# Kernel tuning notes

Measured on AMD Instinct MI355X. Metric: run time of the kernel, lower is better.

Reference implementation:

```python
import jax, jax.numpy as jnp
import numpy as np

EMBED_DIM = 1024
NUM_HEADS = 16
HEAD_DIM = EMBED_DIM // NUM_HEADS
B, S = 2, 2048
NEG = -1e20


def setup_inputs() -> dict:
    key = jax.random.key(0)
    ks = jax.random.split(key, 8)
    scale = 0.02
    return {
        "query": jax.random.normal(ks[0], (B, S, EMBED_DIM), jnp.float32),
        "keys": jax.random.normal(ks[1], (B, S, EMBED_DIM), jnp.float32),
        "values": jax.random.normal(ks[2], (B, S, EMBED_DIM), jnp.float32),
        "mask": jax.random.randint(ks[3], (1, 1, S, S), 0, 2, jnp.int32),
        "Wq": jax.random.normal(ks[4], (EMBED_DIM, EMBED_DIM), jnp.float32) * scale,
        "Wk": jax.random.normal(ks[5], (EMBED_DIM, EMBED_DIM), jnp.float32) * scale,
        "Wv": jax.random.normal(ks[6], (EMBED_DIM, EMBED_DIM), jnp.float32) * scale,
        "Wo": jax.random.normal(ks[7], (EMBED_DIM, EMBED_DIM), jnp.float32) * scale,
        "bo": jnp.zeros((EMBED_DIM,), jnp.float32),
    }


def reference(query, keys, values, mask, Wq, Wk, Wv, Wo, bo):
    N, Lq, _ = query.shape
    Lk = keys.shape[1]
    # torch nn.Linear: y = x @ W.T  (bias=False for Q/K/V)
    Q = (query @ Wq.T).reshape(N, Lq, NUM_HEADS, HEAD_DIM)
    K = (keys @ Wk.T).reshape(N, Lk, NUM_HEADS, HEAD_DIM)
    V = (values @ Wv.T).reshape(N, Lk, NUM_HEADS, HEAD_DIM)
    # NOTE: source scales by sqrt(embed_dim), not sqrt(head_dim) — kept faithful.
    energy = jnp.einsum("nqhd,nkhd->nhqk", Q, K) / jnp.sqrt(
        jnp.asarray(EMBED_DIM, Q.dtype)
    )
    energy = jnp.where(mask == 0, jnp.asarray(NEG, energy.dtype), energy)
    attention = jax.nn.softmax(energy, axis=3)
    out = jnp.einsum("nhqk,nkhd->nqhd", attention, V).reshape(N, Lq, EMBED_DIM)
    return out @ Wo.T + bo
```

## Files before the change

### kernel.cpp

```cpp
#include <hip/hip_runtime.h>
#include <stdint.h>

typedef __bf16 bf16;
typedef __bf16 bf16x4 __attribute__((ext_vector_type(4)));
typedef __bf16 bf16x8 __attribute__((ext_vector_type(8)));
typedef float f32x4 __attribute__((ext_vector_type(4)));
typedef float f32x16 __attribute__((ext_vector_type(16)));

#define MFMA16(a, b, c) __builtin_amdgcn_mfma_f32_16x16x32_bf16((a), (b), (c), 0, 0, 0)
#define MFMA32(a, b, c) __builtin_amdgcn_mfma_f32_32x32x16_bf16((a), (b), (c), 0, 0, 0)

__device__ __forceinline__ void gload16(const bf16* g, bf16* l) {
    __builtin_amdgcn_global_load_lds(
        (const __attribute__((address_space(1))) void*)g,
        (__attribute__((address_space(3))) void*)l, 16, 0, 0);
}

__global__ __launch_bounds__(256) void cvt_kernel(
    const float* __restrict__ q, const float* __restrict__ k, const float* __restrict__ v,
    const float* __restrict__ wq, const float* __restrict__ wk,
    const float* __restrict__ wv, const float* __restrict__ wo,
    bf16* __restrict__ qb, bf16* __restrict__ kb, bf16* __restrict__ vb,
    bf16* __restrict__ wqb, bf16* __restrict__ wkb, bf16* __restrict__ wvb,
    bf16* __restrict__ wob)
{
    int z = blockIdx.z;
    const float* src; bf16* dst; int n;
    switch (z) {
        case 0:  src = q;  dst = qb;  n = 4194304; break;
        case 1:  src = k;  dst = kb;  n = 4194304; break;
        case 2:  src = v;  dst = vb;  n = 4194304; break;
        case 3:  src = wq; dst = wqb; n = 1048576; break;
        case 4:  src = wk; dst = wkb; n = 1048576; break;
        case 5:  src = wv; dst = wvb; n = 1048576; break;
        default: src = wo; dst = wob; n = 1048576; break;
    }
    int i = (blockIdx.x * 256 + threadIdx.x) * 8;
    if (i >= n) return;
    float4 f0 = *(const float4*)(src + i);
    float4 f1 = *(const float4*)(src + i + 4);
    bf16x8 o;
    o[0] = (bf16)f0.x; o[1] = (bf16)f0.y; o[2] = (bf16)f0.z; o[3] = (bf16)f0.w;
    o[4] = (bf16)f1.x; o[5] = (bf16)f1.y; o[6] = (bf16)f1.z; o[7] = (bf16)f1.w;
    *(bf16x8*)(dst + i) = o;
}

__global__ __launch_bounds__(256) void maskpack_kernel(
    const int* __restrict__ mask, unsigned long long* __restrict__ maskb)
{
    int gid  = blockIdx.x * 256 + threadIdx.x;
    int word = gid >> 6;
    int lane = gid & 63;
    int row = word >> 5, wc = word & 31;
    int mv = mask[row * 2048 + wc * 64 + lane];
    unsigned long long bits = __ballot(mv != 0);
    if (lane == 0) maskb[word] = bits;
}

template <int OUTMODE, int MT>
__global__ __launch_bounds__(256) void gemm_kernel(
    const bf16* __restrict__ A0, const bf16* __restrict__ A1, const bf16* __restrict__ A2,
    const bf16* __restrict__ B0, const bf16* __restrict__ B1, const bf16* __restrict__ B2,
    bf16* __restrict__ C0, bf16* __restrict__ C1, bf16* __restrict__ C2,
    const float* __restrict__ bias, float* __restrict__ outf)
{
    constexpr int MI = (MT == 128) ? 4 : 2;

    const int z = blockIdx.z;
    const bf16* A = (z == 0) ? A0 : (z == 1) ? A1 : A2;
    const bf16* B = (z == 0) ? B0 : (z == 1) ? B1 : B2;

    __shared__ bf16 At[MT * 32];
    __shared__ bf16 Bt[128 * 32];

    const int tid  = threadIdx.x;
    const int lane = tid & 63;
    const int wave = tid >> 6;
    const int quad = lane >> 4;
    const int l16  = lane & 15;
    const int wm = (wave >> 1) * (MT / 2);
    const int wn = (wave & 1) * 64;
    const int m0 = blockIdx.y * MT;
    const int n0 = blockIdx.x * 128;

    const int lrow = lane >> 2;
    const int lcol = (lane & 3) * 8;

    f32x4 acc[MI][4] = {};

    const bf16* Ag = A + (size_t)(m0 + lrow) * 1024 + lcol;
    const bf16* Bg = B + (size_t)(n0 + lrow) * 1024 + lcol;

    for (int k0 = 0; k0 < 1024; k0 += 32) {
        __syncthreads();
        if constexpr (MT == 128) {
#pragma unroll
            for (int j = 0; j < 2; ++j)
                gload16(Ag + (size_t)(wave * 32 + j * 16) * 1024 + k0,
                        At + (wave * 32 + j * 16) * 32);
        } else {
            gload16(Ag + (size_t)(wave * 16) * 1024 + k0, At + (wave * 16) * 32);
        }
#pragma unroll
        for (int j = 0; j < 2; ++j)
            gload16(Bg + (size_t)(wave * 32 + j * 16) * 1024 + k0,
                    Bt + (wave * 32 + j * 16) * 32);
        __syncthreads();

        bf16x8 af[MI], bg[4];
#pragma unroll
        for (int i = 0; i < MI; ++i)
            af[i] = *(const bf16x8*)(At + (wm + i * 16 + l16) * 32 + quad * 8);
#pragma unroll
        for (int j = 0; j < 4; ++j)
            bg[j] = *(const bf16x8*)(Bt + (wn + j * 16 + l16) * 32 + quad * 8);
#pragma unroll
        for (int i = 0; i < MI; ++i)
#pragma unroll
            for (int j = 0; j < 4; ++j)
                acc[i][j] = MFMA16(af[i], bg[j], acc[i][j]);
    }

    if constexpr (OUTMODE == 0) {
        bf16* C = (z == 0) ? C0 : (z == 1) ? C1 : C2;
        const float cs = (z == 0) ? 0.03125f : 1.0f;
#pragma unroll
        for (int i = 0; i < MI; ++i)
#pragma unroll
            for (int j = 0; j < 4; ++j) {
                int row = m0 + wm + i * 16 + quad * 4;
                int col = n0 + wn + j * 16 + l16;
#pragma unroll
                for (int r = 0; r < 4; ++r)
                    C[(row + r) * 1024 + col] = (bf16)(acc[i][j][r] * cs);
            }
    } else {
#pragma unroll
        for (int j = 0; j < 4; ++j) {
            int col = n0 + wn + j * 16 + l16;
            float bj = bias[col];
#pragma unroll
            for (int i = 0; i < MI; ++i) {
                int row = m0 + wm + i * 16 + quad * 4;
#pragma unroll
                for (int r = 0; r < 4; ++r)
                    outf[(row + r) * 1024 + col] = acc[i][j][r] + bj;
            }
        }
    }
}

__global__ __launch_bounds__(256) void transpose_kernel(const bf16* __restrict__ V,
                                                        bf16* __restrict__ Vt)
{
    __shared__ bf16 t[64][72];
    const int tid = threadIdx.x;
    const int b  = blockIdx.z;
    const int s0 = blockIdx.x * 64;
    const int d0 = blockIdx.y * 64;
#pragma unroll
    for (int c = 0; c < 2; ++c) {
        int qq = c * 256 + tid;
        int row = qq >> 3, col = (qq & 7) * 8;
        *(uint4*)(&t[row][col]) =
            *(const uint4*)(V + (size_t)(b * 2048 + s0 + row) * 1024 + d0 + col);
    }
    __syncthreads();
#pragma unroll
    for (int c = 0; c < 2; ++c) {
        int qq = c * 256 + tid;
        int drow = qq >> 3, scol = (qq & 7) * 8;
        bf16x8 o;
#pragma unroll
        for (int j = 0; j < 8; ++j) o[j] = t[scol + j][drow];
        *(bf16x8*)(Vt + (size_t)(b * 1024 + d0 + drow) * 2048 + s0 + scol) = o;
    }
}

__global__ __launch_bounds__(256) void flash_kernel(
    const bf16* __restrict__ Q, const bf16* __restrict__ K, const bf16* __restrict__ Vt,
    const unsigned long long* __restrict__ maskb, bf16* __restrict__ O)
{
    __shared__ bf16 Kl[64 * 64];
    __shared__ bf16 Vl[64 * 64];
    __shared__ bf16 Pl[128 * 72];

    const int tid  = threadIdx.x;
    const int lane = tid & 63;
    const int wave = tid >> 6;
    const int l32  = lane & 31;
    const int hl   = lane >> 5;
    const int l7   = lane & 7;
    const int b  = blockIdx.z;
    const int h  = blockIdx.y;
    const int q0 = blockIdx.x * 128;
    const int qt = q0 + wave * 32;

    const bf16* Qb = Q + (size_t)(b * 2048 + qt + l32) * 1024 + h * 64 + hl * 8;
    bf16x8 qf[4];
#pragma unroll
    for (int ks = 0; ks < 4; ++ks) qf[ks] = *(const bf16x8*)(Qb + ks * 16);

    bf16x8 ones;
#pragma unroll
    for (int j = 0; j < 8; ++j) ones[j] = (bf16)1.0f;

    f32x16 acc[2] = {};
    f32x16 lacc = {};

    const int dmarow = lane >> 3;
    const int dmacol = (l7 ^ dmarow) * 8;
    const bf16* Kg = K + (size_t)(b * 2048 + wave * 16 + dmarow) * 1024 + h * 64 + dmacol;
    const bf16* Vg = Vt + (size_t)((b * 16 + h) * 64 + wave * 16 + dmarow) * 2048 + dmacol;
    bf16* Kw = Kl + (wave * 16) * 64;
    bf16* Vw = Vl + (wave * 16) * 64;
    const unsigned long long* Mg = maskb + (size_t)(qt + l32) * 32;

    bf16* Pq = Pl + (wave * 32 + l32) * 72;

    for (int kt = 0; kt < 2048; kt += 64) {
        unsigned long long mw = Mg[kt >> 6];
        __syncthreads();
        gload16(Kg + (size_t)kt * 1024,       Kw);
        gload16(Kg + (size_t)(kt + 8) * 1024, Kw + 8 * 64);
        gload16(Vg + kt,                      Vw);
        gload16(Vg + kt + 8 * 2048,           Vw + 8 * 64);
        __syncthreads();

#pragma unroll
        for (int t = 0; t < 2; ++t) {
            f32x16 s = {};
#pragma unroll
            for (int ks = 0; ks < 4; ++ks) {
                bf16x8 ka = *(const bf16x8*)(Kl + (t * 32 + l32) * 64 +
                                             (((ks * 2 + hl) ^ l7) * 8));
                s = MFMA32(ka, qf[ks], s);
            }
            unsigned long long mwt = mw >> (t * 32 + 4 * hl);
#pragma unroll
            for (int g = 0; g < 4; ++g) {
                bf16x4 pv;
#pragma unroll
                for (int r = 0; r < 4; ++r) {
                    bool keep = (mwt >> (8 * g + r)) & 1ULL;
                    float e = __expf(s[g * 4 + r]);
                    pv[r] = keep ? (bf16)e : (bf16)0.0f;
                }
                *(bf16x4*)(Pq + t * 32 + 4 * hl + 8 * g) = pv;
            }
        }

        bf16x8 pa[4];
#pragma unroll
        for (int ks = 0; ks < 4; ++ks)
            pa[ks] = *(const bf16x8*)(Pq + ks * 16 + hl * 8);
#pragma unroll
        for (int dt = 0; dt < 2; ++dt)
#pragma unroll
            for (int ks = 0; ks < 4; ++ks) {
                bf16x8 vb = *(const bf16x8*)(Vl + (dt * 32 + l32) * 64 +
                                             (((ks * 2 + hl) ^ l7) * 8));
                acc[dt] = MFMA32(pa[ks], vb, acc[dt]);
            }
#pragma unroll
        for (int ks = 0; ks < 4; ++ks)
            lacc = MFMA32(pa[ks], ones, lacc);
    }

    const size_t obase = (size_t)(b * 2048 + qt) * 1024 + h * 64;
#pragma unroll
    for (int g = 0; g < 4; ++g)
#pragma unroll
        for (int r = 0; r < 4; ++r) {
            int qr = 4 * hl + 8 * g + r;
            float inv = 1.0f / lacc[g * 4 + r];
            O[obase + (size_t)qr * 1024 + l32]      = (bf16)(acc[0][g * 4 + r] * inv);
            O[obase + (size_t)qr * 1024 + 32 + l32] = (bf16)(acc[1][g * 4 + r] * inv);
        }
}

extern "C" void kernel_launch(void* const* d_in, const int* in_sizes, int n_in,
                              void* d_out, int out_size, void* d_ws, size_t ws_size,
                              hipStream_t stream)
{
    const float* q  = (const float*)d_in[0];
    const float* k  = (const float*)d_in[1];
    const float* v  = (const float*)d_in[2];
    const int* mask = (const int*)d_in[3];
    const float* wq = (const float*)d_in[4];
    const float* wk = (const float*)d_in[5];
    const float* wv = (const float*)d_in[6];
    const float* wo = (const float*)d_in[7];
    const float* bo = (const float*)d_in[8];
    float* out = (float*)d_out;

    char* p = (char*)d_ws;
    auto alloc = [&](size_t bytes) {
        char* r = p;
        p += (bytes + 255) & ~(size_t)255;
        return r;
    };
    const size_t SB = (size_t)4096 * 1024 * 2;
    const size_t WB = (size_t)1024 * 1024 * 2;
    bf16* qb  = (bf16*)alloc(SB);
    bf16* kb  = (bf16*)alloc(SB);
    bf16* vb  = (bf16*)alloc(SB);
    bf16* wqb = (bf16*)alloc(WB);
    bf16* wkb = (bf16*)alloc(WB);
    bf16* wvb = (bf16*)alloc(WB);
    bf16* wob = (bf16*)alloc(WB);
    bf16* Qp  = (bf16*)alloc(SB);
    bf16* Kp  = (bf16*)alloc(SB);
    bf16* Vp  = (bf16*)alloc(SB);
    bf16* Vtp = (bf16*)alloc(SB);
    bf16* Ob  = (bf16*)alloc(SB);
    unsigned long long* maskb = (unsigned long long*)alloc(2048 * 32 * 8);

    cvt_kernel<<<dim3(2048, 1, 7), 256, 0, stream>>>(
        q, k, v, wq, wk, wv, wo, qb, kb, vb, wqb, wkb, wvb, wob);

    maskpack_kernel<<<dim3(16384), 256, 0, stream>>>(mask, maskb);

    gemm_kernel<0, 128><<<dim3(8, 32, 3), 256, 0, stream>>>(
        qb, kb, vb, wqb, wkb, wvb, Qp, Kp, Vp, nullptr, nullptr);

    transpose_kernel<<<dim3(32, 16, 2), 256, 0, stream>>>(Vp, Vtp);

    flash_kernel<<<dim3(16, 16, 2), 256, 0, stream>>>(Qp, Kp, Vtp, maskb, Ob);

    gemm_kernel<1, 64><<<dim3(8, 64, 1), 256, 0, stream>>>(
        Ob, nullptr, nullptr, wob, nullptr, nullptr,
        nullptr, nullptr, nullptr, bo, out);
}
```

Before: 255.3 us.

## Fuse V transpose into GEMM epilogue and split flash keys across waves

The V projection GEMM now writes its output directly in transposed layout, which removes the separate transpose kernel and its intermediate buffer. The flash kernel shrinks its query tile to 64 rows and doubles the grid. Each pair of waves now splits every 64-key block into two 32-key halves, and the partial outputs and row sums are reduced through shared memory at the end. The Q scale folds in log2(e) so exp2f can replace __expf, and launch bounds request higher occupancy. The cost is extra K/V tile loads per query, an end-of-kernel shared-memory reduction, and uncoalesced 4-element stores in the transposed epilogue.

```diff
diff --git a/kernel.cpp b/kernel.cpp
--- a/kernel.cpp
+++ b/kernel.cpp
@@ -122,18 +122,33 @@
     }
 
     if constexpr (OUTMODE == 0) {
-        bf16* C = (z == 0) ? C0 : (z == 1) ? C1 : C2;
-        const float cs = (z == 0) ? 0.03125f : 1.0f;
-#pragma unroll
-        for (int i = 0; i < MI; ++i)
-#pragma unroll
-            for (int j = 0; j < 4; ++j) {
-                int row = m0 + wm + i * 16 + quad * 4;
-                int col = n0 + wn + j * 16 + l16;
-#pragma unroll
-                for (int r = 0; r < 4; ++r)
-                    C[(row + r) * 1024 + col] = (bf16)(acc[i][j][r] * cs);
-            }
+        if (z == 2) {
+#pragma unroll
+            for (int i = 0; i < MI; ++i)
+#pragma unroll
+                for (int j = 0; j < 4; ++j) {
+                    int row = m0 + wm + i * 16 + quad * 4;
+                    int col = n0 + wn + j * 16 + l16;
+                    bf16x4 pv;
+#pragma unroll
+                    for (int r = 0; r < 4; ++r) pv[r] = (bf16)acc[i][j][r];
+                    *(bf16x4*)(C2 + ((size_t)((row >> 11) * 1024 + col)) * 2048 +
+                               (row & 2047)) = pv;
+                }
+        } else {
+            bf16* C = (z == 0) ? C0 : C1;
+            const float cs = (z == 0) ? 0.04508422f : 1.0f;
+#pragma unroll
+            for (int i = 0; i < MI; ++i)
+#pragma unroll
+                for (int j = 0; j < 4; ++j) {
+                    int row = m0 + wm + i * 16 + quad * 4;
+                    int col = n0 + wn + j * 16 + l16;
+#pragma unroll
+                    for (int r = 0; r < 4; ++r)
+                        C[(row + r) * 1024 + col] = (bf16)(acc[i][j][r] * cs);
+                }
+        }
     } else {
 #pragma unroll
         for (int j = 0; j < 4; ++j) {
@@ -150,40 +165,16 @@
     }
 }
 
-__global__ __launch_bounds__(256) void transpose_kernel(const bf16* __restrict__ V,
-                                                        bf16* __restrict__ Vt)
-{
-    __shared__ bf16 t[64][72];
-    const int tid = threadIdx.x;
-    const int b  = blockIdx.z;
-    const int s0 = blockIdx.x * 64;
-    const int d0 = blockIdx.y * 64;
-#pragma unroll
-    for (int c = 0; c < 2; ++c) {
-        int qq = c * 256 + tid;
-        int row = qq >> 3, col = (qq & 7) * 8;
-        *(uint4*)(&t[row][col]) =
-            *(const uint4*)(V + (size_t)(b * 2048 + s0 + row) * 1024 + d0 + col);
-    }
-    __syncthreads();
-#pragma unroll
-    for (int c = 0; c < 2; ++c) {
-        int qq = c * 256 + tid;
-        int drow = qq >> 3, scol = (qq & 7) * 8;
-        bf16x8 o;
-#pragma unroll
-        for (int j = 0; j < 8; ++j) o[j] = t[scol + j][drow];
-        *(bf16x8*)(Vt + (size_t)(b * 1024 + d0 + drow) * 2048 + s0 + scol) = o;
-    }
-}
-
-__global__ __launch_bounds__(256) void flash_kernel(
+__global__ __launch_bounds__(256, 4) void flash_kernel(
     const bf16* __restrict__ Q, const bf16* __restrict__ K, const bf16* __restrict__ Vt,
     const unsigned long long* __restrict__ maskb, bf16* __restrict__ O)
 {
-    __shared__ bf16 Kl[64 * 64];
-    __shared__ bf16 Vl[64 * 64];
-    __shared__ bf16 Pl[128 * 72];
+    __shared__ char smem[8192 + 8192 + 9216];
+    bf16* Kl = (bf16*)smem;
+    bf16* Vl = (bf16*)(smem + 8192);
+    bf16* Pl = (bf16*)(smem + 16384);
+    float* Obuf = (float*)smem;
+    float* Lbuf = (float*)(smem + 16384);
 
     const int tid  = threadIdx.x;
     const int lane = tid & 63;
@@ -191,10 +182,12 @@
     const int l32  = lane & 31;
     const int hl   = lane >> 5;
     const int l7   = lane & 7;
+    const int qtw  = wave & 1;
+    const int kh   = wave >> 1;
     const int b  = blockIdx.z;
     const int h  = blockIdx.y;
-    const int q0 = blockIdx.x * 128;
-    const int qt = q0 + wave * 32;
+    const int q0 = blockIdx.x * 64;
+    const int qt = q0 + qtw * 32;
 
     const bf16* Qb = Q + (size_t)(b * 2048 + qt + l32) * 1024 + h * 64 + hl * 8;
     bf16x8 qf[4];
@@ -216,7 +209,7 @@
     bf16* Vw = Vl + (wave * 16) * 64;
     const unsigned long long* Mg = maskb + (size_t)(qt + l32) * 32;
 
-    bf16* Pq = Pl + (wave * 32 + l32) * 72;
+    bf16* Pq = Pl + wave * (32 * 36) + l32 * 36;
 
     for (int kt = 0; kt < 2048; kt += 64) {
         unsigned long long mw = Mg[kt >> 6];
@@ -227,56 +220,79 @@
         gload16(Vg + kt + 8 * 2048,           Vw + 8 * 64);
         __syncthreads();
 
-#pragma unroll
-        for (int t = 0; t < 2; ++t) {
-            f32x16 s = {};
-#pragma unroll
-            for (int ks = 0; ks < 4; ++ks) {
-                bf16x8 ka = *(const bf16x8*)(Kl + (t * 32 + l32) * 64 +
-                                             (((ks * 2 + hl) ^ l7) * 8));
-                s = MFMA32(ka, qf[ks], s);
-            }
-            unsigned long long mwt = mw >> (t * 32 + 4 * hl);
-#pragma unroll
-            for (int g = 0; g < 4; ++g) {
-                bf16x4 pv;
-#pragma unroll
-                for (int r = 0; r < 4; ++r) {
-                    bool keep = (mwt >> (8 * g + r)) & 1ULL;
-                    float e = __expf(s[g * 4 + r]);
-                    pv[r] = keep ? (bf16)e : (bf16)0.0f;
-                }
-                *(bf16x4*)(Pq + t * 32 + 4 * hl + 8 * g) = pv;
-            }
-        }
-
-        bf16x8 pa[4];
-#pragma unroll
-        for (int ks = 0; ks < 4; ++ks)
+        f32x16 s = {};
+#pragma unroll
+        for (int ks = 0; ks < 4; ++ks) {
+            bf16x8 ka = *(const bf16x8*)(Kl + (kh * 32 + l32) * 64 +
+                                         (((ks * 2 + hl) ^ l7) * 8));
+            s = MFMA32(ka, qf[ks], s);
+        }
+
+        unsigned long long mq = mw >> (kh * 32 + 4 * hl);
+#pragma unroll
+        for (int g = 0; g < 4; ++g) {
+            bf16x4 pv;
+#pragma unroll
+            for (int r = 0; r < 4; ++r) {
+                bool keep = (mq >> (8 * g + r)) & 1ULL;
+                float e = exp2f(s[g * 4 + r]);
+                pv[r] = keep ? (bf16)e : (bf16)0.0f;
+            }
+            *(bf16x4*)(Pq + 4 * hl + 8 * g) = pv;
+        }
+
+        bf16x8 pa[2];
+#pragma unroll
+        for (int ks = 0; ks < 2; ++ks)
             pa[ks] = *(const bf16x8*)(Pq + ks * 16 + hl * 8);
 #pragma unroll
         for (int dt = 0; dt < 2; ++dt)
 #pragma unroll
-            for (int ks = 0; ks < 4; ++ks) {
+            for (int ks = 0; ks < 2; ++ks) {
                 bf16x8 vb = *(const bf16x8*)(Vl + (dt * 32 + l32) * 64 +
-                                             (((ks * 2 + hl) ^ l7) * 8));
+                                             (((kh * 4 + ks * 2 + hl) ^ l7) * 8));
                 acc[dt] = MFMA32(pa[ks], vb, acc[dt]);
             }
-#pragma unroll
-        for (int ks = 0; ks < 4; ++ks)
-            lacc = MFMA32(pa[ks], ones, lacc);
-    }
-
-    const size_t obase = (size_t)(b * 2048 + qt) * 1024 + h * 64;
-#pragma unroll
-    for (int g = 0; g < 4; ++g)
-#pragma unroll
-        for (int r = 0; r < 4; ++r) {
-            int qr = 4 * hl + 8 * g + r;
-            float inv = 1.0f / lacc[g * 4 + r];
-            O[obase + (size_t)qr * 1024 + l32]      = (bf16)(acc[0][g * 4 + r] * inv);
-            O[obase + (size_t)qr * 1024 + 32 + l32] = (bf16)(acc[1][g * 4 + r] * inv);
-        }
+        lacc = MFMA32(pa[0], ones, lacc);
+        lacc = MFMA32(pa[1], ones, lacc);
+    }
+
+    __syncthreads();
+    if (kh == 1) {
+        float* ob = Obuf + (qtw * 32) * 64;
+#pragma unroll
+        for (int g = 0; g < 4; ++g)
+#pragma unroll
+            for (int r = 0; r < 4; ++r) {
+                int qr = 4 * hl + 8 * g + r;
+                ob[qr * 64 + l32]      = acc[0][g * 4 + r];
+                ob[qr * 64 + 32 + l32] = acc[1][g * 4 + r];
+            }
+        if (l32 == 0) {
+#pragma unroll
+            for (int g = 0; g < 4; ++g)
+#pragma unroll
+                for (int r = 0; r < 4; ++r)
+                    Lbuf[qtw * 32 + 4 * hl + 8 * g + r] = lacc[g * 4 + r];
+        }
+    }
+    __syncthreads();
+    if (kh == 0) {
+        const float* ob = Obuf + (qtw * 32) * 64;
+        const size_t obase = (size_t)(b * 2048 + qt) * 1024 + h * 64;
+#pragma unroll
+        for (int g = 0; g < 4; ++g)
+#pragma unroll
+            for (int r = 0; r < 4; ++r) {
+                int qr = 4 * hl + 8 * g + r;
+                float l = lacc[g * 4 + r] + Lbuf[qtw * 32 + qr];
+                float inv = 1.0f / l;
+                float o0 = acc[0][g * 4 + r] + ob[qr * 64 + l32];
+                float o1 = acc[1][g * 4 + r] + ob[qr * 64 + 32 + l32];
+                O[obase + (size_t)qr * 1024 + l32]      = (bf16)(o0 * inv);
+                O[obase + (size_t)qr * 1024 + 32 + l32] = (bf16)(o1 * inv);
+            }
+    }
 }
 
 extern "C" void kernel_launch(void* const* d_in, const int* in_sizes, int n_in,
@@ -311,7 +327,6 @@
     bf16* wob = (bf16*)alloc(WB);
     bf16* Qp  = (bf16*)alloc(SB);
     bf16* Kp  = (bf16*)alloc(SB);
-    bf16* Vp  = (bf16*)alloc(SB);
     bf16* Vtp = (bf16*)alloc(SB);
     bf16* Ob  = (bf16*)alloc(SB);
     unsigned long long* maskb = (unsigned long long*)alloc(2048 * 32 * 8);
@@ -322,11 +337,9 @@
     maskpack_kernel<<<dim3(16384), 256, 0, stream>>>(mask, maskb);
 
     gemm_kernel<0, 128><<<dim3(8, 32, 3), 256, 0, stream>>>(
-        qb, kb, vb, wqb, wkb, wvb, Qp, Kp, Vp, nullptr, nullptr);
-
-    transpose_kernel<<<dim3(32, 16, 2), 256, 0, stream>>>(Vp, Vtp);
-
-    flash_kernel<<<dim3(16, 16, 2), 256, 0, stream>>>(Qp, Kp, Vtp, maskb, Ob);
+        qb, kb, vb, wqb, wkb, wvb, Qp, Kp, Vtp, nullptr, nullptr);
+
+    flash_kernel<<<dim3(32, 16, 2), 256, 0, stream>>>(Qp, Kp, Vtp, maskb, Ob);
 
     gemm_kernel<1, 64><<<dim3(8, 64, 1), 256, 0, stream>>>(
         Ob, nullptr, nullptr, wob, nullptr, nullptr,
```

Result: slower. 271.5 us (+6.3%).

## Use 32x32 MFMA with swizzled BK=64 GEMM tiles and fuse V transpose into epilogue

Applied to the files above, without the earlier changes.

Reworks the projection GEMM to use 32x32x16 MFMA on 64-wide K tiles, with an XOR-swizzled LDS layout that reduces bank conflicts and halves the number of K-loop barriers. The V projection epilogue now writes directly in transposed layout, which removes the separate transpose kernel and its extra global read and write. The Q scale is folded to include log2(e) so the flash kernel can use exp2f instead of __expf. The transposed store writes 4-element vectors along the sequence dimension, which may coalesce less well than the old row-major stores.

```diff
diff --git a/kernel.cpp b/kernel.cpp
--- a/kernel.cpp
+++ b/kernel.cpp
@@ -7,7 +7,6 @@
 typedef float f32x4 __attribute__((ext_vector_type(4)));
 typedef float f32x16 __attribute__((ext_vector_type(16)));
 
-#define MFMA16(a, b, c) __builtin_amdgcn_mfma_f32_16x16x32_bf16((a), (b), (c), 0, 0, 0)
 #define MFMA32(a, b, c) __builtin_amdgcn_mfma_f32_32x32x16_bf16((a), (b), (c), 0, 0, 0)
 
 __device__ __forceinline__ void gload16(const bf16* g, bf16* l) {
@@ -64,116 +63,115 @@
     bf16* __restrict__ C0, bf16* __restrict__ C1, bf16* __restrict__ C2,
     const float* __restrict__ bias, float* __restrict__ outf)
 {
-    constexpr int MI = (MT == 128) ? 4 : 2;
+    constexpr int MTw = MT / 64;
 
     const int z = blockIdx.z;
     const bf16* A = (z == 0) ? A0 : (z == 1) ? A1 : A2;
     const bf16* B = (z == 0) ? B0 : (z == 1) ? B1 : B2;
 
-    __shared__ bf16 At[MT * 32];
-    __shared__ bf16 Bt[128 * 32];
+    __shared__ bf16 At[MT * 64];
+    __shared__ bf16 Bt[128 * 64];
 
     const int tid  = threadIdx.x;
     const int lane = tid & 63;
     const int wave = tid >> 6;
-    const int quad = lane >> 4;
-    const int l16  = lane & 15;
+    const int l32  = lane & 31;
+    const int hl   = lane >> 5;
+    const int l7   = lane & 7;
     const int wm = (wave >> 1) * (MT / 2);
     const int wn = (wave & 1) * 64;
     const int m0 = blockIdx.y * MT;
     const int n0 = blockIdx.x * 128;
 
-    const int lrow = lane >> 2;
-    const int lcol = (lane & 3) * 8;
-
-    f32x4 acc[MI][4] = {};
-
-    const bf16* Ag = A + (size_t)(m0 + lrow) * 1024 + lcol;
-    const bf16* Bg = B + (size_t)(n0 + lrow) * 1024 + lcol;
-
-    for (int k0 = 0; k0 < 1024; k0 += 32) {
+    const int dmarow = lane >> 3;
+    const int dmacol = ((lane & 7) ^ dmarow) * 8;
+    const bf16* Ag = A + (size_t)(m0 + dmarow) * 1024 + dmacol;
+    const bf16* Bg = B + (size_t)(n0 + dmarow) * 1024 + dmacol;
+
+    f32x16 acc[MTw][2] = {};
+
+    for (int k0 = 0; k0 < 1024; k0 += 64) {
         __syncthreads();
-        if constexpr (MT == 128) {
-#pragma unroll
-            for (int j = 0; j < 2; ++j)
-                gload16(Ag + (size_t)(wave * 32 + j * 16) * 1024 + k0,
-                        At + (wave * 32 + j * 16) * 32);
+#pragma unroll
+        for (int j = 0; j < MT / 32; ++j) {
+            int rb = wave * (MT / 4) + j * 8;
+            gload16(Ag + (size_t)rb * 1024 + k0, At + rb * 64);
+        }
+#pragma unroll
+        for (int j = 0; j < 4; ++j) {
+            int rb = wave * 32 + j * 8;
+            gload16(Bg + (size_t)rb * 1024 + k0, Bt + rb * 64);
+        }
+        __syncthreads();
+
+#pragma unroll
+        for (int ks = 0; ks < 4; ++ks) {
+            const int cidx = (((ks * 2 + hl) ^ l7) * 8);
+            bf16x8 af[MTw], bg[2];
+#pragma unroll
+            for (int mt = 0; mt < MTw; ++mt)
+                af[mt] = *(const bf16x8*)(At + (wm + mt * 32 + l32) * 64 + cidx);
+#pragma unroll
+            for (int nt = 0; nt < 2; ++nt)
+                bg[nt] = *(const bf16x8*)(Bt + (wn + nt * 32 + l32) * 64 + cidx);
+#pragma unroll
+            for (int mt = 0; mt < MTw; ++mt)
+#pragma unroll
+                for (int nt = 0; nt < 2; ++nt)
+                    acc[mt][nt] = MFMA32(af[mt], bg[nt], acc[mt][nt]);
+        }
+    }
+
+    if constexpr (OUTMODE == 0) {
+        if (z == 2) {
+#pragma unroll
+            for (int mt = 0; mt < MTw; ++mt)
+#pragma unroll
+                for (int nt = 0; nt < 2; ++nt)
+#pragma unroll
+                    for (int g = 0; g < 4; ++g) {
+                        int row = m0 + wm + mt * 32 + 4 * hl + 8 * g;
+                        int col = n0 + wn + nt * 32 + l32;
+                        bf16x4 pv;
+#pragma unroll
+                        for (int r = 0; r < 4; ++r) pv[r] = (bf16)acc[mt][nt][g * 4 + r];
+                        *(bf16x4*)(C2 + ((size_t)((row >> 11) * 1024 + col)) * 2048 +
+                                   (row & 2047)) = pv;
+                    }
         } else {
-            gload16(Ag + (size_t)(wave * 16) * 1024 + k0, At + (wave * 16) * 32);
-        }
-#pragma unroll
-        for (int j = 0; j < 2; ++j)
-            gload16(Bg + (size_t)(wave * 32 + j * 16) * 1024 + k0,
-                    Bt + (wave * 32 + j * 16) * 32);
-        __syncthreads();
-
-        bf16x8 af[MI], bg[4];
-#pragma unroll
-        for (int i = 0; i < MI; ++i)
-            af[i] = *(const bf16x8*)(At + (wm + i * 16 + l16) * 32 + quad * 8);
-#pragma unroll
-        for (int j = 0; j < 4; ++j)
-            bg[j] = *(const bf16x8*)(Bt + (wn + j * 16 + l16) * 32 + quad * 8);
-#pragma unroll
-        for (int i = 0; i < MI; ++i)
-#pragma unroll
-            for (int j = 0; j < 4; ++j)
-                acc[i][j] = MFMA16(af[i], bg[j], acc[i][j]);
-    }
-
-    if constexpr (OUTMODE == 0) {
-        bf16* C = (z == 0) ? C0 : (z == 1) ? C1 : C2;
-        const float cs = (z == 0) ? 0.03125f : 1.0f;
-#pragma unroll
-        for (int i = 0; i < MI; ++i)
-#pragma unroll
-            for (int j = 0; j < 4; ++j) {
-                int row = m0 + wm + i * 16 + quad * 4;
-                int col = n0 + wn + j * 16 + l16;
-#pragma unroll
-                for (int r = 0; r < 4; ++r)
-                    C[(row + r) * 1024 + col] = (bf16)(acc[i][j][r] * cs);
-            }
+            bf16* C = (z == 0) ? C0 : C1;
+            const float cs = (z == 0) ? 0.04508422f : 1.0f;
+#pragma unroll
+            for (int mt = 0; mt < MTw; ++mt)
+#pragma unroll
+                for (int nt = 0; nt < 2; ++nt) {
+                    int col = n0 + wn + nt * 32 + l32;
+#pragma unroll
+                    for (int g = 0; g < 4; ++g) {
+                        int row = m0 + wm + mt * 32 + 4 * hl + 8 * g;
+#pragma unroll
+                        for (int r = 0; r < 4; ++r)
+                            C[(size_t)(row + r) * 1024 + col] =
+                                (bf16)(acc[mt][nt][g * 4 + r] * cs);
+                    }
+                }
+        }
     } else {
 #pragma unroll
-        for (int j = 0; j < 4; ++j) {
-            int col = n0 + wn + j * 16 + l16;
+        for (int nt = 0; nt < 2; ++nt) {
+            int col = n0 + wn + nt * 32 + l32;
             float bj = bias[col];
 #pragma unroll
-            for (int i = 0; i < MI; ++i) {
-                int row = m0 + wm + i * 16 + quad * 4;
-#pragma unroll
-                for (int r = 0; r < 4; ++r)
-                    outf[(row + r) * 1024 + col] = acc[i][j][r] + bj;
-            }
-        }
-    }
-}
-
-__global__ __launch_bounds__(256) void transpose_kernel(const bf16* __restrict__ V,
-                                                        bf16* __restrict__ Vt)
-{
-    __shared__ bf16 t[64][72];
-    const int tid = threadIdx.x;
-    const int b  = blockIdx.z;
-    const int s0 = blockIdx.x * 64;
-    const int d0 = blockIdx.y * 64;
-#pragma unroll
-    for (int c = 0; c < 2; ++c) {
-        int qq = c * 256 + tid;
-        int row = qq >> 3, col = (qq & 7) * 8;
-        *(uint4*)(&t[row][col]) =
-            *(const uint4*)(V + (size_t)(b * 2048 + s0 + row) * 1024 + d0 + col);
-    }
-    __syncthreads();
-#pragma unroll
-    for (int c = 0; c < 2; ++c) {
-        int qq = c * 256 + tid;
-        int drow = qq >> 3, scol = (qq & 7) * 8;
-        bf16x8 o;
-#pragma unroll
-        for (int j = 0; j < 8; ++j) o[j] = t[scol + j][drow];
-        *(bf16x8*)(Vt + (size_t)(b * 1024 + d0 + drow) * 2048 + s0 + scol) = o;
+            for (int mt = 0; mt < MTw; ++mt)
+#pragma unroll
+                for (int g = 0; g < 4; ++g) {
+                    int row = m0 + wm + mt * 32 + 4 * hl + 8 * g;
+#pragma unroll
+                    for (int r = 0; r < 4; ++r)
+                        outf[(size_t)(row + r) * 1024 + col] =
+                            acc[mt][nt][g * 4 + r] + bj;
+                }
+        }
     }
 }
 
@@ -243,7 +241,7 @@
 #pragma unroll
                 for (int r = 0; r < 4; ++r) {
                     bool keep = (mwt >> (8 * g + r)) & 1ULL;
-                    float e = __expf(s[g * 4 + r]);
+                    float e = exp2f(s[g * 4 + r]);
                     pv[r] = keep ? (bf16)e : (bf16)0.0f;
                 }
                 *(bf16x4*)(Pq + t * 32 + 4 * hl + 8 * g) = pv;
@@ -311,7 +309,6 @@
     bf16* wob = (bf16*)alloc(WB);
     bf16* Qp  = (bf16*)alloc(SB);
     bf16* Kp  = (bf16*)alloc(SB);
-    bf16* Vp  = (bf16*)alloc(SB);
     bf16* Vtp = (bf16*)alloc(SB);
     bf16* Ob  = (bf16*)alloc(SB);
     unsigned long long* maskb = (unsigned long long*)alloc(2048 * 32 * 8);
@@ -322,9 +319,7 @@
     maskpack_kernel<<<dim3(16384), 256, 0, stream>>>(mask, maskb);
 
     gemm_kernel<0, 128><<<dim3(8, 32, 3), 256, 0, stream>>>(
-        qb, kb, vb, wqb, wkb, wvb, Qp, Kp, Vp, nullptr, nullptr);
-
-    transpose_kernel<<<dim3(32, 16, 2), 256, 0, stream>>>(Vp, Vtp);
+        qb, kb, vb, wqb, wkb, wvb, Qp, Kp, Vtp, nullptr, nullptr);
 
     flash_kernel<<<dim3(16, 16, 2), 256, 0, stream>>>(Qp, Kp, Vtp, maskb, Ob);
 
```

Result: slower. 272.4 us (+6.7%).
